# Optimization experiments

Hardware: AMD Instinct MI355X
Metric: run time of the kernel (lower is better)

## Reference

```python
import jax, jax.numpy as jnp
import numpy as np

MEM_LEN = 8


def _conv(x, w, b, stride=1):
    y = jax.lax.conv_general_dilated(x, w, (stride, stride), 'VALID',
                                     dimension_numbers=('NCHW', 'OIHW', 'NCHW'))
    return y + b[None, :, None, None]


def _maxpool3s2(x):
    return jax.lax.reduce_window(x, -jnp.inf, jax.lax.max,
                                 (1, 1, 3, 3), (1, 1, 2, 2), 'VALID')


def _relu(x):
    return jax.nn.relu(x)


def setup_inputs() -> dict:
    key = jax.random.key(0)
    ks = jax.random.split(key, 32)

    def w(i, shape):
        fan_in = float(np.prod(shape[1:]))
        return jax.random.normal(ks[i], shape, jnp.float32) * np.float32(1.0 / np.sqrt(fan_in))

    def bias(i, n):
        return jax.random.normal(ks[i], (n,), jnp.float32) * np.float32(0.01)

    return {
        'x': jax.random.normal(ks[0], (1, 287, 287, 3), jnp.float32),
        'z_reg': jax.random.normal(ks[1], (MEM_LEN, 256, 16), jnp.float32) * 0.1,
        'z_cls': jax.random.normal(ks[2], (MEM_LEN, 256, 16), jnp.float32) * 0.1,
        'bb_w1': w(3, (96, 3, 11, 11)),  'bb_b1': bias(4, 96),
        'bb_w2': w(5, (256, 96, 5, 5)),  'bb_b2': bias(6, 256),
        'bb_w3': w(7, (384, 256, 3, 3)), 'bb_b3': bias(8, 384),
        'bb_w4': w(9, (384, 384, 3, 3)), 'bb_b4': bias(10, 384),
        'bb_w5': w(11, (256, 384, 3, 3)), 'bb_b5': bias(12, 256),
        'wr': w(13, (256, 256, 3, 3)), 'br': bias(14, 256),   # conv_reg2 (conv_search of loc)
        'wc': w(15, (256, 256, 3, 3)), 'bc': bias(16, 256),   # conv_cls2 (conv_search of cls)
        'rh_w1': w(17, (256, 256, 1, 1)), 'rh_b1': bias(18, 256),
        'rh_w2': w(19, (20, 256, 1, 1)),  'rh_b2': bias(20, 20),
        'ch_w1': w(21, (256, 256, 1, 1)), 'ch_b1': bias(22, 256),
        'ch_w2': w(23, (10, 256, 1, 1)),  'ch_b2': bias(24, 10),
        'anc0': jax.random.normal(ks[25], (MEM_LEN, 2205), jnp.float32) * 10.0,
        'anc1': jax.random.normal(ks[26], (MEM_LEN, 2205), jnp.float32) * 10.0,
        'anc2': jax.random.uniform(ks[27], (MEM_LEN, 2205), jnp.float32) * 80.0 + 20.0,
        'anc3': jax.random.uniform(ks[28], (MEM_LEN, 2205), jnp.float32) * 80.0 + 20.0,
    }


def reference(x, z_reg, z_cls,
              bb_w1, bb_b1, bb_w2, bb_b2, bb_w3, bb_b3, bb_w4, bb_b4, bb_w5, bb_b5,
              wr, br, wc, bc,
              rh_w1, rh_b1, rh_w2, rh_b2, ch_w1, ch_b1, ch_w2, ch_b2,
              anc0, anc1, anc2, anc3):
    # Backbone (AlexNet features, BN folded into biases)
    xp = jnp.transpose(x, (0, 3, 1, 2))                     # (1,3,287,287)
    h = _relu(_maxpool3s2(_conv(xp, bb_w1, bb_b1, 2)))      # (1,96,69,69)
    h = _relu(_maxpool3s2(_conv(h, bb_w2, bb_b2)))          # (1,256,32,32)
    h = _relu(_conv(h, bb_w3, bb_b3))                       # (1,384,30,30)
    h = _relu(_conv(h, bb_w4, bb_b4))                       # (1,384,28,28)
    xf = _conv(h, bb_w5, bb_b5)                             # (1,256,26,26)

    c_x = _relu(_conv(xf, wr, br))                          # conv_reg2 -> (1,256,24,24)
    r_x = _relu(_conv(xf, wc, bc))                          # conv_cls2 -> (1,256,24,24)

    def unfold44(t):                                        # (1,256,24,24) -> (256,16,441)
        p = jax.lax.conv_general_dilated_patches(
            t.reshape(256, 1, 24, 24), (4, 4), (1, 1), 'VALID',
            dimension_numbers=('NCHW', 'OIHW', 'NCHW'))     # (256,16,21,21)
        return p.reshape(256, 16, 441)

    c_p = unfold44(c_x)
    r_p = unfold44(r_x)

    # Batched cross-correlation over mem_len templates (fuses the original python loop)
    zr = z_reg.reshape(MEM_LEN, 256, 16)
    zc = z_cls.reshape(MEM_LEN, 256, 16)
    reg_corr = jnp.einsum('ckl,mck->mcl', r_p, zr).reshape(MEM_LEN, 256, 21, 21)
    cls_corr = jnp.einsum('ckl,mck->mcl', c_p, zc).reshape(MEM_LEN, 256, 21, 21)

    cls = _conv(_relu(_conv(cls_corr, ch_w1, ch_b1)), ch_w2, ch_b2)   # (M,10,21,21)
    reg = _conv(_relu(_conv(reg_corr, rh_w1, rh_b1)), rh_w2, rh_b2)   # (M,20,21,21)

    score = jax.nn.softmax(cls.reshape(MEM_LEN, 2, -1), axis=1)       # (M,2,2205)
    delta = reg.reshape(MEM_LEN, 4, -1)                               # (M,4,2205)

    d0 = delta[:, 0, :] * anc2 + anc0
    d1 = delta[:, 1, :] * anc3 + anc1
    d2 = jnp.exp(delta[:, 2, :]) * anc2
    d3 = jnp.exp(delta[:, 3, :]) * anc3
    return (d0, d1, d2, d3, score[:, 1, :])
```

## Files before the change

kernel.cpp:

```cpp
#include <hip/hip_runtime.h>
#include <math.h>

#define TPB 256
static inline int cdiv(int a, int b) { return (a + b - 1) / b; }

typedef short bf8 __attribute__((ext_vector_type(8)));
typedef float f4 __attribute__((ext_vector_type(4)));

__device__ inline float b2f(unsigned short u) {
    union { unsigned int i; float f; } v; v.i = ((unsigned int)u) << 16; return v.f;
}
__device__ inline short f2b(float f) {
    union { float f; unsigned int u; } v; v.f = f;
    unsigned int r = v.u + 0x7FFF + ((v.u >> 16) & 1);
    return (short)(r >> 16);
}

#define OW1   0
#define OW2   67584
#define OW3   722944
#define OW4   1607680
#define OW5   2934784
#define OWRC  3819520
#define OWH1  4999168
#define OZT   5130240
#define OWH2  5195776
#define OBIAS 5203456
#define OACT1 5205504
#define OP1   7062368
#define OACTB 7521472
#define OXF   9520064
#define OCRC  9695168

#define ACT2_OFF  0
#define POOL2_OFF 1083648
#define ACT3_OFF  1347840
#define ACT4_OFF  1695488

__global__ __launch_bounds__(256) void wprep_k(
        const float* __restrict__ bb_w1, const float* __restrict__ bb_w2,
        const float* __restrict__ bb_w3, const float* __restrict__ bb_w4,
        const float* __restrict__ bb_w5,
        const float* __restrict__ wr, const float* __restrict__ wc,
        const float* __restrict__ ch_w1, const float* __restrict__ rh_w1,
        const float* __restrict__ ch_w2, const float* __restrict__ rh_w2,
        const float* __restrict__ z_cls, const float* __restrict__ z_reg,
        const float* __restrict__ br, const float* __restrict__ bc,
        const float* __restrict__ chb1, const float* __restrict__ rhb1,
        const float* __restrict__ x,
        short* __restrict__ W, float* __restrict__ biasf,
        short* __restrict__ xb) {
    __shared__ float lds[3465];
    int bid = blockIdx.x;
    int t = threadIdx.x;

    if (bid < 1792) {
        const float* src;
        short* dst;
        int C, K2, Ot, KwC, orow;
        if (bid < 384)       { int o = bid;        C = 256; K2 = 9;  src = bb_w3 + (size_t)o * 2304; dst = W + OW3;  Ot = 384; KwC = 768;  orow = o; }
        else if (bid < 768)  { int o = bid - 384;  C = 384; K2 = 9;  src = bb_w4 + (size_t)o * 3456; dst = W + OW4;  Ot = 384; KwC = 1152; orow = o; }
        else if (bid < 1024) { int o = bid - 768;  C = 384; K2 = 9;  src = bb_w5 + (size_t)o * 3456; dst = W + OW5;  Ot = 256; KwC = 1152; orow = o; }
        else if (bid < 1280) { int o = bid - 1024; C = 256; K2 = 9;  src = wr    + (size_t)o * 2304; dst = W + OWRC; Ot = 512; KwC = 768;  orow = o; }
        else if (bid < 1536) { int o = bid - 1280; C = 256; K2 = 9;  src = wc    + (size_t)o * 2304; dst = W + OWRC; Ot = 512; KwC = 768;  orow = o + 256; }
        else                 { int o = bid - 1536; C = 96;  K2 = 25; src = bb_w2 + (size_t)o * 2400; dst = W + OW2;  Ot = 256; KwC = 512;  orow = o; }

        int n = C * K2;
        int Cp = C + 1;
        if (K2 == 9) {
            for (int i = t; i < n; i += 256) {
                int kk = i % 9, c = i / 9;
                lds[kk * Cp + c] = src[i];
            }
            __syncthreads();
#pragma unroll
            for (int kk = 0; kk < 9; ++kk) {
                int ki = kk / 3, kj = kk % 3;
                short* rowb = dst + ((size_t)ki * Ot + orow) * KwC + kj * C;
                for (int c = t; c < C; c += 256)
                    rowb[c] = f2b(lds[kk * Cp + c]);
            }
        } else {
            for (int i = t; i < n; i += 256) {
                int kk = i % 25, c = i / 25;
                lds[kk * Cp + c] = src[i];
            }
            __syncthreads();
            for (int kk = 0; kk < 25; ++kk) {
                int ki = kk / 5, kj = kk % 5;
                short* rowb = dst + ((size_t)ki * Ot + orow) * KwC + kj * C;
                if (t < C) rowb[t] = f2b(lds[kk * Cp + t]);
            }
            if (t < 160) {
                int ki = t / 32, kp = 480 + (t & 31);
                dst[((size_t)ki * Ot + orow) * KwC + kp] = 0;
            }
        }
        return;
    }

    int fidx = (bid - 1792) * 256 + t;
    if (fidx < 67584) {
        int k = fidx & 63, o = (fidx >> 6) % 96, ki = fidx / (64 * 96);
        float v = 0.f;
        if (k < 33) v = bb_w1[o * 363 + (k % 3) * 121 + ki * 11 + (k / 3)];
        W[fidx] = f2b(v);
    } else if (fidx < 198656) {
        int i = fidx - 67584;
        const float* src = (i < 65536) ? ch_w1 : rh_w1;
        W[OWH1 + i] = f2b(src[i & 65535]);
    } else if (fidx < 206336) {
        int i = fidx - 198656;
        int o = i >> 8, c = i & 255;
        float v = (o < 10) ? ch_w2[o * 256 + c] : rh_w2[(o - 10) * 256 + c];
        W[OWH2 + i] = f2b(v);
    } else if (fidx < 271872) {
        int i = fidx - 206336;
        const float* src = (i < 32768) ? z_cls : z_reg;
        int j = i & 32767;
        int c = j & 255, k = (j >> 8) & 15, m = j >> 12;
        W[OZT + i] = f2b(src[m * 4096 + c * 16 + k]);
    } else if (fidx < 272896) {
        int i = fidx - 271872;
        const float* src = (i < 256) ? br : (i < 512) ? bc : (i < 768) ? chb1 : rhb1;
        biasf[i] = src[i & 255];
    } else {
        int i = fidx - 272896;
        if (i < 247107) xb[i] = f2b(x[i]);
    }
}

template <int BKC>
__global__ __launch_bounds__(256) void gemm_k(
        const short* __restrict__ in, const short* __restrict__ wt,
        const float* __restrict__ bias, short* __restrict__ out,
        int M, int N, int Wo, int CinW, int Cin,
        int S, int SPR, int aWrap, int bWrap, int KwCp,
        int relu, int msplit, int wsec, int bsec, int nt) {
    constexpr int BK = BKC * 32;
    constexpr int LDW = BK + 8;
    constexpr int CPR = BK / 8;
    constexpr int RPR = 256 / CPR;
    __shared__ short sa[2][64 * LDW];
    __shared__ short sb[2][64 * LDW];

    int bid = blockIdx.x;
    int m0 = (bid / nt) * 64, n0 = (bid % nt) * 64;
    int t = threadIdx.x;
    int lane = t & 63;
    int wid = t >> 6, wm = wid >> 1, wn = wid & 1;
    int sec = (m0 >= msplit) ? 1 : 0;
    const short* wts = wt + (size_t)sec * wsec;
    const float* bs = bias + sec * bsec;

    int rql = t / CPR;
    int ch8 = (t % CPR) * 8;

    const short* pA[BKC];
    const short* pB[BKC];
#pragma unroll
    for (int q = 0; q < BKC; ++q) {
        int mr = m0 + q * RPR + rql; if (mr > M - 1) mr = M - 1;
        int oy = mr / Wo, ox = mr - oy * Wo;
        pA[q] = in + (size_t)oy * CinW + (size_t)ox * Cin + ch8;
        int nr = n0 + q * RPR + rql; if (nr > N - 1) nr = N - 1;
        pB[q] = wts + (size_t)nr * KwCp + ch8;
    }
    int swb = rql * LDW + ch8;

    int arow = (wm * 32 + (lane & 15)) * LDW + (lane >> 4) * 8;
    int brow = (wn * 32 + (lane & 15)) * LDW + (lane >> 4) * 8;

    f4 acc[2][2] = {};
    bf8 va[BKC], vb[BKC];
    int srow = 0;

#define LOAD_STEP()                                                           \
    do {                                                                      \
        _Pragma("unroll")                                                     \
        for (int q = 0; q < BKC; ++q) {                                       \
            va[q] = *(const bf8*)pA[q];                                       \
            vb[q] = *(const bf8*)pB[q];                                       \
        }                                                                     \
        if (++srow == SPR) {                                                  \
            srow = 0;                                                         \
            _Pragma("unroll")                                                 \
            for (int q = 0; q < BKC; ++q) { pA[q] += aWrap; pB[q] += bWrap; } \
        } else {                                                              \
            _Pragma("unroll")                                                 \
            for (int q = 0; q < BKC; ++q) { pA[q] += BK; pB[q] += BK; }       \
        }                                                                     \
    } while (0)

    LOAD_STEP();
#pragma unroll
    for (int q = 0; q < BKC; ++q) {
        *(bf8*)&sa[0][swb + q * (RPR * LDW)] = va[q];
        *(bf8*)&sb[0][swb + q * (RPR * LDW)] = vb[q];
    }
    __syncthreads();

    for (int s = 0; s < S; ++s) {
        int cur = s & 1;
        bool pre = (s + 1 < S);
        if (pre) LOAD_STEP();
        const short* A = sa[cur];
        const short* B = sb[cur];
#pragma unroll
        for (int kc = 0; kc < BKC; ++kc) {
            bf8 a0 = *(const bf8*)&A[arow + kc * 32];
            bf8 a1 = *(const bf8*)&A[arow + 16 * LDW + kc * 32];
            bf8 b0 = *(const bf8*)&B[brow + kc * 32];
            bf8 b1 = *(const bf8*)&B[brow + 16 * LDW + kc * 32];
            acc[0][0] = __builtin_amdgcn_mfma_f32_16x16x32_bf16(a0, b0, acc[0][0], 0, 0, 0);
            acc[0][1] = __builtin_amdgcn_mfma_f32_16x16x32_bf16(a0, b1, acc[0][1], 0, 0, 0);
            acc[1][0] = __builtin_amdgcn_mfma_f32_16x16x32_bf16(a1, b0, acc[1][0], 0, 0, 0);
            acc[1][1] = __builtin_amdgcn_mfma_f32_16x16x32_bf16(a1, b1, acc[1][1], 0, 0, 0);
        }
        if (pre) {
            int nb = cur ^ 1;
#pragma unroll
            for (int q = 0; q < BKC; ++q) {
                *(bf8*)&sa[nb][swb + q * (RPR * LDW)] = va[q];
                *(bf8*)&sb[nb][swb + q * (RPR * LDW)] = vb[q];
            }
        }
        __syncthreads();
    }
#undef LOAD_STEP

#pragma unroll
    for (int i = 0; i < 2; ++i) {
#pragma unroll
        for (int j = 0; j < 2; ++j) {
            int gm_base = m0 + wm * 32 + i * 16 + (lane >> 4) * 4;
            int gn = n0 + wn * 32 + j * 16 + (lane & 15);
            if (gn < N) {
                float bv = bs[gn];
#pragma unroll
                for (int r = 0; r < 4; ++r) {
                    int gm = gm_base + r;
                    if (gm < M) {
                        float v = acc[i][j][r] + bv;
                        if (relu) v = fmaxf(v, 0.f);
                        out[(size_t)gm * N + gn] = f2b(v);
                    }
                }
            }
        }
    }
}

__global__ void pool_k(const short* __restrict__ in, short* __restrict__ out,
                       int C8, int Win, int Ho) {
    int idx = blockIdx.x * blockDim.x + threadIdx.x;
    int total = Ho * Ho * C8;
    if (idx >= total) return;
    int c8 = idx % C8;
    int p = idx / C8;
    int oy = p / Ho, ox = p % Ho;
    int C = C8 * 8;
    float mx[8];
#pragma unroll
    for (int e = 0; e < 8; ++e) mx[e] = -INFINITY;
#pragma unroll
    for (int ki = 0; ki < 3; ++ki)
#pragma unroll
        for (int kj = 0; kj < 3; ++kj) {
            const bf8 v = *(const bf8*)(in + ((size_t)(oy * 2 + ki) * Win + ox * 2 + kj) * C + c8 * 8);
#pragma unroll
            for (int e = 0; e < 8; ++e) mx[e] = fmaxf(mx[e], b2f((unsigned short)v[e]));
        }
    bf8 o;
#pragma unroll
    for (int e = 0; e < 8; ++e) o[e] = f2b(fmaxf(mx[e], 0.f));
    *(bf8*)(out + (size_t)p * C + c8 * 8) = o;
}

__global__ void dwcorr_k(const short* __restrict__ crcb, const short* __restrict__ zt,
                         short* __restrict__ corr) {
    int idx = blockIdx.x * blockDim.x + threadIdx.x;
    if (idx >= 2 * 903168) return;
    int half = idx / 903168;
    int r = idx - half * 903168;
    int c = r & 255;
    int l = (r >> 8) % 441;
    int mb = r / (441 * 256);
    int y = l / 21, xx = l % 21;
    const short* ip = crcb + half * 256 + (size_t)(y * 24 + xx) * 512 + c;
    const short* zp = zt + half * 32768 + mb * 4096 + c;
    float acc = 0.f;
#pragma unroll
    for (int ki = 0; ki < 4; ++ki)
#pragma unroll
        for (int kj = 0; kj < 4; ++kj)
            acc = fmaf(b2f((unsigned short)ip[(ki * 24 + kj) * 512]),
                       b2f((unsigned short)zp[(ki * 4 + kj) * 256]), acc);
    corr[((size_t)(half * 3584 + mb * 441 + l)) * 256 + c] = f2b(acc);
}

__global__ void head2epi_k(const short* __restrict__ hid, const short* __restrict__ wh2,
                           const float* __restrict__ chb2, const float* __restrict__ rhb2,
                           const float* __restrict__ a0, const float* __restrict__ a1,
                           const float* __restrict__ a2, const float* __restrict__ a3,
                           float* __restrict__ out) {
    const int Ntot = 8 * 2205;
    int idx = blockIdx.x * blockDim.x + threadIdx.x;
    if (idx >= 3 * Ntot) return;
    int g = idx / Ntot;
    int r = idx - g * Ntot;
    int m = r / 2205, j = r % 2205;
    int a = j / 441, pos = j % 441;
    int ml = m * 441 + pos;
    const short* h = hid + (size_t)((g == 0) ? ml : 3584 + ml) * 256;
    int row0, row1;
    float acc0, acc1;
    if (g == 0)      { row0 = a;      row1 = 5 + a;  acc0 = chb2[a];      acc1 = chb2[5 + a];  }
    else if (g == 1) { row0 = 10 + a; row1 = 15 + a; acc0 = rhb2[a];      acc1 = rhb2[5 + a];  }
    else             { row0 = 20 + a; row1 = 25 + a; acc0 = rhb2[10 + a]; acc1 = rhb2[15 + a]; }
    const short* w0 = wh2 + row0 * 256;
    const short* w1 = wh2 + row1 * 256;
    for (int c = 0; c < 256; c += 8) {
        bf8 hv = *(const bf8*)(h + c);
        bf8 w0v = *(const bf8*)(w0 + c);
        bf8 w1v = *(const bf8*)(w1 + c);
#pragma unroll
        for (int e = 0; e < 8; ++e) {
            float hf = b2f((unsigned short)hv[e]);
            acc0 = fmaf(hf, b2f((unsigned short)w0v[e]), acc0);
            acc1 = fmaf(hf, b2f((unsigned short)w1v[e]), acc1);
        }
    }
    if (g == 0) {
        out[4 * Ntot + r] = 1.f / (1.f + expf(acc0 - acc1));
    } else if (g == 1) {
        out[0 * Ntot + r] = fmaf(acc0, a2[r], a0[r]);
        out[1 * Ntot + r] = fmaf(acc1, a3[r], a1[r]);
    } else {
        out[2 * Ntot + r] = expf(acc0) * a2[r];
        out[3 * Ntot + r] = expf(acc1) * a3[r];
    }
}

extern "C" void kernel_launch(void* const* d_in, const int* in_sizes, int n_in,
                              void* d_out, int out_size, void* d_ws, size_t ws_size,
                              hipStream_t stream) {
    const float* x     = (const float*)d_in[0];
    const float* z_reg = (const float*)d_in[1];
    const float* z_cls = (const float*)d_in[2];
    const float* bb_w1 = (const float*)d_in[3];
    const float* bb_b1 = (const float*)d_in[4];
    const float* bb_w2 = (const float*)d_in[5];
    const float* bb_b2 = (const float*)d_in[6];
    const float* bb_w3 = (const float*)d_in[7];
    const float* bb_b3 = (const float*)d_in[8];
    const float* bb_w4 = (const float*)d_in[9];
    const float* bb_b4 = (const float*)d_in[10];
    const float* bb_w5 = (const float*)d_in[11];
    const float* bb_b5 = (const float*)d_in[12];
    const float* wr    = (const float*)d_in[13];
    const float* br    = (const float*)d_in[14];
    const float* wc    = (const float*)d_in[15];
    const float* bc    = (const float*)d_in[16];
    const float* rh_w1 = (const float*)d_in[17];
    const float* rh_b1 = (const float*)d_in[18];
    const float* rh_w2 = (const float*)d_in[19];
    const float* rh_b2 = (const float*)d_in[20];
    const float* ch_w1 = (const float*)d_in[21];
    const float* ch_b1 = (const float*)d_in[22];
    const float* ch_w2 = (const float*)d_in[23];
    const float* ch_b2 = (const float*)d_in[24];
    const float* anc0  = (const float*)d_in[25];
    const float* anc1  = (const float*)d_in[26];
    const float* anc2  = (const float*)d_in[27];
    const float* anc3  = (const float*)d_in[28];

    short* sws  = (short*)d_ws;
    short* W    = sws;
    float* biasf = (float*)(sws + OBIAS);
    short* act1 = sws + OACT1;
    short* pool1 = sws + OP1;
    short* actB = sws + OACTB;
    short* xb   = actB;
    short* act2 = actB + ACT2_OFF;
    short* pool2 = actB + POOL2_OFF;
    short* act3 = actB + ACT3_OFF;
    short* act4 = actB + ACT4_OFF;
    short* corr = actB;
    short* xf   = sws + OXF;
    short* crcb = sws + OCRC;
    short* hid  = act1;

    const int BIG = 1 << 30;

    wprep_k<<<1792 + 2032, 256, 0, stream>>>(
        bb_w1, bb_w2, bb_w3, bb_w4, bb_w5, wr, wc, ch_w1, rh_w1, ch_w2, rh_w2,
        z_cls, z_reg, br, bc, ch_b1, rh_b1, x, W, biasf, xb);

    gemm_k<2><<<302 * 2, 256, 0, stream>>>(
        xb, W + OW1, bb_b1, act1,
        19321, 96, 139, 1722, 6,
        11, 1, 861, 6144, 64, 0, BIG, 0, 0, 2);
    pool_k<<<cdiv(69 * 69 * 12, TPB), TPB, 0, stream>>>(act1, pool1, 12, 139, 69);

    gemm_k<4><<<67 * 4, 256, 0, stream>>>(
        pool1, W + OW2, bb_b2, act2,
        4225, 256, 65, 6624, 96,
        20, 4, 6240, 130688, 512, 0, BIG, 0, 0, 4);
    pool_k<<<cdiv(32 * 32 * 32, TPB), TPB, 0, stream>>>(act2, pool2, 32, 65, 32);

    gemm_k<4><<<15 * 6, 256, 0, stream>>>(
        pool2, W + OW3, bb_b3, act3,
        900, 384, 30, 8192, 256,
        18, 6, 7552, 294272, 768, 1, BIG, 0, 0, 6);

    gemm_k<4><<<13 * 6, 256, 0, stream>>>(
        act3, W + OW4, bb_b4, act4,
        784, 384, 28, 11520, 384,
        27, 9, 10496, 441344, 1152, 1, BIG, 0, 0, 6);

    gemm_k<4><<<11 * 4, 256, 0, stream>>>(
        act4, W + OW5, bb_b5, xf,
        676, 256, 26, 10752, 384,
        27, 9, 9728, 293888, 1152, 0, BIG, 0, 0, 4);

    gemm_k<4><<<9 * 8, 256, 0, stream>>>(
        xf, W + OWRC, biasf, crcb,
        576, 512, 24, 6656, 256,
        18, 6, 6016, 392576, 768, 1, BIG, 0, 0, 8);

    dwcorr_k<<<cdiv(2 * 903168, TPB), TPB, 0, stream>>>(crcb, W + OZT, corr);

    gemm_k<4><<<112 * 4, 256, 0, stream>>>(
        corr, W + OWH1, biasf + 512, hid,
        7112, 256, 7112, 0, 256,
        2, 2, 0, 0, 256, 1, 3584, 65536, 256, 4);

    head2epi_k<<<cdiv(3 * 8 * 2205, TPB), TPB, 0, stream>>>(
        hid, W + OWH2, ch_b2, rh_b2, anc0, anc1, anc2, anc3, (float*)d_out);
}
```

Before: 165.4 us.

## Load GEMM weight fragments straight from global into registers, drop B shared tile

The weight (B) operand no longer goes through a double-buffered shared-memory tile. Each wave loads its own MFMA B fragments directly from global memory into registers at the start of every k-step, while A keeps the shared-memory double buffer. This halves LDS usage and removes the B shared-memory stores and reads, and launch bounds now request 4 blocks per CU. In exchange, B loads are issued without prefetch, so their latency sits just ahead of the MFMAs, and each weight element is fetched by two waves instead of one.

```diff
diff --git a/kernel.cpp b/kernel.cpp
--- a/kernel.cpp
+++ b/kernel.cpp
@@ -131,7 +131,7 @@
 }
 
 template <int BKC>
-__global__ __launch_bounds__(256) void gemm_k(
+__global__ __launch_bounds__(256, 4) void gemm_k(
         const short* __restrict__ in, const short* __restrict__ wt,
         const float* __restrict__ bias, short* __restrict__ out,
         int M, int N, int Wo, int CinW, int Cin,
@@ -142,7 +142,6 @@
     constexpr int CPR = BK / 8;
     constexpr int RPR = 256 / CPR;
     __shared__ short sa[2][64 * LDW];
-    __shared__ short sb[2][64 * LDW];
 
     int bid = blockIdx.x;
     int m0 = (bid / nt) * 64, n0 = (bid % nt) * 64;
@@ -157,77 +156,77 @@
     int ch8 = (t % CPR) * 8;
 
     const short* pA[BKC];
-    const short* pB[BKC];
 #pragma unroll
     for (int q = 0; q < BKC; ++q) {
         int mr = m0 + q * RPR + rql; if (mr > M - 1) mr = M - 1;
         int oy = mr / Wo, ox = mr - oy * Wo;
         pA[q] = in + (size_t)oy * CinW + (size_t)ox * Cin + ch8;
-        int nr = n0 + q * RPR + rql; if (nr > N - 1) nr = N - 1;
-        pB[q] = wts + (size_t)nr * KwCp + ch8;
+    }
+    const short* pBg[2];
+#pragma unroll
+    for (int f = 0; f < 2; ++f) {
+        int nr = n0 + wn * 32 + f * 16 + (lane & 15);
+        if (nr > N - 1) nr = N - 1;
+        pBg[f] = wts + (size_t)nr * KwCp + (lane >> 4) * 8;
     }
     int swb = rql * LDW + ch8;
-
     int arow = (wm * 32 + (lane & 15)) * LDW + (lane >> 4) * 8;
-    int brow = (wn * 32 + (lane & 15)) * LDW + (lane >> 4) * 8;
 
     f4 acc[2][2] = {};
-    bf8 va[BKC], vb[BKC];
-    int srow = 0;
-
-#define LOAD_STEP()                                                           \
+    bf8 va[BKC];
+    int srowA = 0, srowB = 0;
+
+#define LOAD_A()                                                              \
     do {                                                                      \
         _Pragma("unroll")                                                     \
-        for (int q = 0; q < BKC; ++q) {                                       \
-            va[q] = *(const bf8*)pA[q];                                       \
-            vb[q] = *(const bf8*)pB[q];                                       \
-        }                                                                     \
-        if (++srow == SPR) {                                                  \
-            srow = 0;                                                         \
+        for (int q = 0; q < BKC; ++q) va[q] = *(const bf8*)pA[q];             \
+        if (++srowA == SPR) {                                                 \
+            srowA = 0;                                                        \
             _Pragma("unroll")                                                 \
-            for (int q = 0; q < BKC; ++q) { pA[q] += aWrap; pB[q] += bWrap; } \
+            for (int q = 0; q < BKC; ++q) pA[q] += aWrap;                     \
         } else {                                                              \
             _Pragma("unroll")                                                 \
-            for (int q = 0; q < BKC; ++q) { pA[q] += BK; pB[q] += BK; }       \
+            for (int q = 0; q < BKC; ++q) pA[q] += BK;                        \
         }                                                                     \
     } while (0)
 
-    LOAD_STEP();
-#pragma unroll
-    for (int q = 0; q < BKC; ++q) {
+    LOAD_A();
+#pragma unroll
+    for (int q = 0; q < BKC; ++q)
         *(bf8*)&sa[0][swb + q * (RPR * LDW)] = va[q];
-        *(bf8*)&sb[0][swb + q * (RPR * LDW)] = vb[q];
-    }
     __syncthreads();
 
     for (int s = 0; s < S; ++s) {
         int cur = s & 1;
         bool pre = (s + 1 < S);
-        if (pre) LOAD_STEP();
+        bf8 breg[BKC][2];
+#pragma unroll
+        for (int q = 0; q < BKC; ++q) {
+            breg[q][0] = *(const bf8*)(pBg[0] + q * 32);
+            breg[q][1] = *(const bf8*)(pBg[1] + q * 32);
+        }
+        if (++srowB == SPR) { srowB = 0; pBg[0] += bWrap; pBg[1] += bWrap; }
+        else                { pBg[0] += BK; pBg[1] += BK; }
+        if (pre) LOAD_A();
         const short* A = sa[cur];
-        const short* B = sb[cur];
 #pragma unroll
         for (int kc = 0; kc < BKC; ++kc) {
             bf8 a0 = *(const bf8*)&A[arow + kc * 32];
             bf8 a1 = *(const bf8*)&A[arow + 16 * LDW + kc * 32];
-            bf8 b0 = *(const bf8*)&B[brow + kc * 32];
-            bf8 b1 = *(const bf8*)&B[brow + 16 * LDW + kc * 32];
-            acc[0][0] = __builtin_amdgcn_mfma_f32_16x16x32_bf16(a0, b0, acc[0][0], 0, 0, 0);
-            acc[0][1] = __builtin_amdgcn_mfma_f32_16x16x32_bf16(a0, b1, acc[0][1], 0, 0, 0);
-            acc[1][0] = __builtin_amdgcn_mfma_f32_16x16x32_bf16(a1, b0, acc[1][0], 0, 0, 0);
-            acc[1][1] = __builtin_amdgcn_mfma_f32_16x16x32_bf16(a1, b1, acc[1][1], 0, 0, 0);
+            acc[0][0] = __builtin_amdgcn_mfma_f32_16x16x32_bf16(a0, breg[kc][0], acc[0][0], 0, 0, 0);
+            acc[0][1] = __builtin_amdgcn_mfma_f32_16x16x32_bf16(a0, breg[kc][1], acc[0][1], 0, 0, 0);
+            acc[1][0] = __builtin_amdgcn_mfma_f32_16x16x32_bf16(a1, breg[kc][0], acc[1][0], 0, 0, 0);
+            acc[1][1] = __builtin_amdgcn_mfma_f32_16x16x32_bf16(a1, breg[kc][1], acc[1][1], 0, 0, 0);
         }
         if (pre) {
             int nb = cur ^ 1;
 #pragma unroll
-            for (int q = 0; q < BKC; ++q) {
+            for (int q = 0; q < BKC; ++q)
                 *(bf8*)&sa[nb][swb + q * (RPR * LDW)] = va[q];
-                *(bf8*)&sb[nb][swb + q * (RPR * LDW)] = vb[q];
-            }
         }
         __syncthreads();
     }
-#undef LOAD_STEP
+#undef LOAD_A
 
 #pragma unroll
     for (int i = 0; i < 2; ++i) {
```

New measurement: 269.5 us. 63.0% more time.
